# Performance work log

Hardware: AMD Instinct MI355X
Metric: run time of the kernel (lower is better)

Reference implementation:

```python
import jax, jax.numpy as jnp
import numpy as np

N_DIALOGS = 60
DIA_LEN = 100
N = N_DIALOGS * DIA_LEN  # 6000 utterances total
D_IN = 512
D_OUT = 512


def setup_inputs() -> dict:
    key = jax.random.key(0)
    k1, k2, k3, k4 = jax.random.split(key, 4)
    inputs = jax.random.normal(k1, (N, D_IN), dtype=jnp.float32)
    # per-dialog lengths (concrete host array; defines static graph structure)
    dia_len = np.full((N_DIALOGS,), DIA_LEN, dtype=np.int64)
    # one-hot speaker mask [N, 1, 2]; qmask[j,0,0]==1 -> speaker0 else speaker1
    sp = jax.random.randint(k2, (N,), 0, 2)
    qmask = jnp.zeros((N, 1, 2), jnp.int64).at[jnp.arange(N), 0, sp].set(1)
    W = jax.random.normal(k3, (D_OUT, D_IN), dtype=jnp.float32) / np.sqrt(D_IN)
    b = jax.random.normal(k4, (D_OUT,), dtype=jnp.float32) * 0.01
    return {"inputs": inputs, "dia_len": dia_len, "qmask": qmask, "W": W, "b": b}


def build_adj(inputs, dia_len, qmask):
    # Vectorized equivalent of message_passing_directed_speaker:
    # adj = I; edge (i,j) iff i,j in same dialog, same speaker, and consecutive
    # among that speaker's utterances; weight = 1 - arccos(clip(cos,-1,1))/pi.
    n = inputs.shape[0]
    dia_len_np = np.asarray(dia_len)
    did = jnp.asarray(np.repeat(np.arange(len(dia_len_np)), dia_len_np))  # dialog id per node
    sp0 = qmask[:, 0, 0] == 1  # True -> speaker0
    cs0 = jnp.cumsum(sp0.astype(jnp.int32))
    cs1 = jnp.cumsum((~sp0).astype(jnp.int32))
    csel = jnp.where(sp0, cs0, cs1)  # running count of own speaker
    idx = jnp.arange(n)
    # j>i, same dialog, same speaker, no same-speaker utterance strictly between
    upper = ((did[None, :] == did[:, None])
             & (sp0[None, :] == sp0[:, None])
             & (csel[None, :] - csel[:, None] == 1)
             & (idx[None, :] > idx[:, None]))
    edge = upper | upper.T
    # pairwise cosine similarity (cossim returns 0 when a norm is 0)
    nrm = jnp.sqrt(jnp.sum(inputs * inputs, axis=-1))  # [N]
    denom = nrm[:, None] * nrm[None, :]
    dots = inputs @ inputs.T  # [N, N]
    cos = jnp.where(denom > 0, dots / jnp.where(denom > 0, denom, 1.0), 0.0)
    cos_safe = jnp.where(edge, jnp.clip(cos, -1.0, 1.0), 0.0)
    w = 1.0 - jnp.arccos(cos_safe) / jnp.pi
    return jnp.where(edge, w, 0.0) + jnp.eye(n, dtype=inputs.dtype)


def reference(inputs, dia_len, qmask, W, b):
    adj = build_adj(inputs, dia_len, qmask)  # [N, N]
    x = adj @ inputs                          # [N, D_IN]
    return x @ W.T + b                        # [N, D_OUT]
```

## Files before the change

### kernel.cpp

```cpp
#include <hip/hip_runtime.h>
#include <hip/hip_bf16.h>

#define N_NODES 6000
#define N_DIA   60
#define DIA     100
#define DDIM    512
#define LDA     520

typedef short short8   __attribute__((ext_vector_type(8)));
typedef float floatx4  __attribute__((ext_vector_type(4)));

__device__ __forceinline__ unsigned short f2bf(float f) {
    unsigned int u = __float_as_uint(f);
    unsigned int r = (u + 0x7fffu + ((u >> 16) & 1u)) >> 16;
    return (unsigned short)r;
}

__device__ __forceinline__ float wave_reduce_sum(float v) {
    #pragma unroll
    for (int off = 32; off > 0; off >>= 1) v += __shfl_xor(v, off, 64);
    return v;
}

__global__ __launch_bounds__(256) void edge_kernel(
    const float* __restrict__ x, const int* __restrict__ qmask,
    const float* __restrict__ W, int* __restrict__ nxt, int* __restrict__ prv,
    float* __restrict__ wn, unsigned short* __restrict__ wbf)
{
    int bid = blockIdx.x;
    int tid = threadIdx.x;
    if (bid >= N_NODES / 4) {
        int base = (bid - N_NODES / 4) * 2048 + tid * 8;
        float4 a = *(const float4*)(W + base);
        float4 b = *(const float4*)(W + base + 4);
        union { unsigned short u[8]; short8 v; } o;
        o.u[0]=f2bf(a.x); o.u[1]=f2bf(a.y); o.u[2]=f2bf(a.z); o.u[3]=f2bf(a.w);
        o.u[4]=f2bf(b.x); o.u[5]=f2bf(b.y); o.u[6]=f2bf(b.z); o.u[7]=f2bf(b.w);
        *(short8*)(wbf + base) = o.v;
        return;
    }
    int wv = tid >> 6, lane = tid & 63;
    int i = bid * 4 + wv;
    int sp = qmask[2 * i];
    int dstart = (i / DIA) * DIA;
    int dend   = dstart + DIA;

    int cand = i + 1 + lane;
    unsigned long long b1 = __ballot(cand < dend && qmask[2 * cand] == sp);
    int j = -1;
    if (b1) j = i + __ffsll(b1);
    else {
        int c2 = i + 65 + lane;
        unsigned long long b2 = __ballot(lane < 35 && c2 < dend && qmask[2 * c2] == sp);
        if (b2) j = i + 64 + __ffsll(b2);
    }
    int candp = i - 1 - lane;
    unsigned long long p1 = __ballot(candp >= dstart && qmask[2 * candp] == sp);
    int p = -1;
    if (p1) p = i - __ffsll(p1);
    else {
        int pc2 = i - 65 - lane;
        unsigned long long p2 = __ballot(lane < 35 && pc2 >= dstart && qmask[2 * pc2] == sp);
        if (p2) p = i - 64 - __ffsll(p2);
    }

    float w = 0.0f;
    if (j >= 0) {
        const float* ri = x + (size_t)i * DDIM + lane * 8;
        const float* rj = x + (size_t)j * DDIM + lane * 8;
        float4 a0 = *(const float4*)(ri);
        float4 a1 = *(const float4*)(ri + 4);
        float4 b0 = *(const float4*)(rj);
        float4 b1 = *(const float4*)(rj + 4);
        float d  = a0.x*b0.x + a0.y*b0.y + a0.z*b0.z + a0.w*b0.w
                 + a1.x*b1.x + a1.y*b1.y + a1.z*b1.z + a1.w*b1.w;
        float ni = a0.x*a0.x + a0.y*a0.y + a0.z*a0.z + a0.w*a0.w
                 + a1.x*a1.x + a1.y*a1.y + a1.z*a1.z + a1.w*a1.w;
        float nj = b0.x*b0.x + b0.y*b0.y + b0.z*b0.z + b0.w*b0.w
                 + b1.x*b1.x + b1.y*b1.y + b1.z*b1.z + b1.w*b1.w;
        d  = wave_reduce_sum(d);
        ni = wave_reduce_sum(ni);
        nj = wave_reduce_sum(nj);
        float dn = ni * nj;
        float c = (dn > 0.0f) ? (d * __frsqrt_rn(dn)) : 0.0f;
        c = fminf(1.0f, fmaxf(-1.0f, c));
        w = 1.0f - acosf(c) * 0.3183098861837907f;
    }
    if (lane == 0) { nxt[i] = j; prv[i] = p; wn[i] = w; }
}

__global__ __launch_bounds__(512) void build_gemm(
    const float* __restrict__ x, const int* __restrict__ nxt,
    const int* __restrict__ prv, const float* __restrict__ wn,
    const unsigned short* __restrict__ wbf, const float* __restrict__ bias,
    float* __restrict__ out)
{
    __shared__ unsigned short As[64 * LDA];
    int tid = threadIdx.x;
    int wv = tid >> 6, lane = tid & 63;
    int m0 = blockIdx.x * 64;

    #pragma unroll 2
    for (int t = 0; t < 8; ++t) {
        int rr = wv * 8 + t;
        int i = m0 + rr;
        unsigned short* dst = As + rr * LDA + lane * 8;
        if (i >= N_NODES) {
            *(short8*)dst = (short8)0;
            continue;
        }
        int j = nxt[i];
        int p = prv[i];
        float wi = (j >= 0) ? wn[i] : 0.0f;
        float wp = (p >= 0) ? wn[p] : 0.0f;
        const float* ri = x + (size_t)i * DDIM + lane * 8;
        float acc[8];
        {
            float4 a = *(const float4*)(ri);
            float4 b = *(const float4*)(ri + 4);
            acc[0]=a.x; acc[1]=a.y; acc[2]=a.z; acc[3]=a.w;
            acc[4]=b.x; acc[5]=b.y; acc[6]=b.z; acc[7]=b.w;
        }
        if (j >= 0) {
            const float* rj = x + (size_t)j * DDIM + lane * 8;
            float4 a = *(const float4*)(rj);
            float4 b = *(const float4*)(rj + 4);
            acc[0]+=wi*a.x; acc[1]+=wi*a.y; acc[2]+=wi*a.z; acc[3]+=wi*a.w;
            acc[4]+=wi*b.x; acc[5]+=wi*b.y; acc[6]+=wi*b.z; acc[7]+=wi*b.w;
        }
        if (p >= 0) {
            const float* rp = x + (size_t)p * DDIM + lane * 8;
            float4 a = *(const float4*)(rp);
            float4 b = *(const float4*)(rp + 4);
            acc[0]+=wp*a.x; acc[1]+=wp*a.y; acc[2]+=wp*a.z; acc[3]+=wp*a.w;
            acc[4]+=wp*b.x; acc[5]+=wp*b.y; acc[6]+=wp*b.z; acc[7]+=wp*b.w;
        }
        union { unsigned short u[8]; short8 v; } o;
        #pragma unroll
        for (int q = 0; q < 8; ++q) o.u[q] = f2bf(acc[q]);
        *(short8*)dst = o.v;
    }
    __syncthreads();

    int n0 = blockIdx.y * 256 + wv * 32;
    int fr = lane & 15;
    int kq = (lane >> 4) * 8;
    floatx4 acc[4][2] = {};
    const unsigned short* As_base = As + fr * LDA + kq;
    const unsigned short* bb = wbf + (size_t)(n0 + fr) * DDIM + kq;

    #pragma unroll 2
    for (int k = 0; k < DDIM; k += 32) {
        short8 af[4], bfv[2];
        #pragma unroll
        for (int ms = 0; ms < 4; ++ms)
            af[ms] = *(const short8*)(As_base + ms * 16 * LDA + k);
        #pragma unroll
        for (int ns = 0; ns < 2; ++ns)
            bfv[ns] = *(const short8*)(bb + (size_t)ns * 16 * DDIM + k);
        #pragma unroll
        for (int ms = 0; ms < 4; ++ms)
            #pragma unroll
            for (int ns = 0; ns < 2; ++ns)
                acc[ms][ns] = __builtin_amdgcn_mfma_f32_16x16x32_bf16(
                    af[ms], bfv[ns], acc[ms][ns], 0, 0, 0);
    }

    int col = lane & 15;
    int rbase = (lane >> 4) * 4;
    #pragma unroll
    for (int ms = 0; ms < 4; ++ms) {
        #pragma unroll
        for (int ns = 0; ns < 2; ++ns) {
            int n = n0 + ns * 16 + col;
            float bv = bias[n];
            #pragma unroll
            for (int r = 0; r < 4; ++r) {
                int m = m0 + ms * 16 + rbase + r;
                if (m < N_NODES)
                    out[(size_t)m * DDIM + n] = acc[ms][ns][r] + bv;
            }
        }
    }
}

extern "C" void kernel_launch(void* const* d_in, const int* in_sizes, int n_in,
                              void* d_out, int out_size, void* d_ws, size_t ws_size,
                              hipStream_t stream) {
    const float* inputs = (const float*)d_in[0];
    const int* qmask   = (const int*)d_in[2];
    const float* W     = (const float*)d_in[3];
    const float* bias  = (const float*)d_in[4];
    float* out = (float*)d_out;

    char* ws = (char*)d_ws;
    unsigned short* wbf = (unsigned short*)ws;
    float* wn  = (float*)(ws + 524288);
    int*   nxt = (int*)(ws + 524288 + 24576);
    int*   prv = (int*)(ws + 524288 + 2 * 24576);

    edge_kernel<<<dim3(N_NODES / 4 + 128), 256, 0, stream>>>(
        inputs, qmask, W, nxt, prv, wn, wbf);
    build_gemm <<<dim3(94, 2),            512, 0, stream>>>(
        inputs, nxt, prv, wn, wbf, bias, out);
}
```

Before: 93.70 us.

## Fuse edge discovery and cosine weights into the build+GEMM kernel

Neighbour finding moves into the build+GEMM kernel: each block stages the speaker flags of its dialog range in shared memory and scans serially for next and previous same-speaker nodes. The cosine weights are then computed inline from the rows already loaded for aggregation. The old edge kernel, which read x for every node and wrote nxt/prv/wn through global memory, shrinks to a small W-cast kernel. This removes a large pass over x and the global round-trip, at the cost of recomputing each edge weight in both directions and doing the serial scans in one wave per block.

```diff
diff --git a/kernel.cpp b/kernel.cpp
--- a/kernel.cpp
+++ b/kernel.cpp
@@ -2,7 +2,6 @@
 #include <hip/hip_bf16.h>
 
 #define N_NODES 6000
-#define N_DIA   60
 #define DIA     100
 #define DDIM    512
 #define LDA     520
@@ -22,85 +21,54 @@
     return v;
 }
 
-__global__ __launch_bounds__(256) void edge_kernel(
+__global__ __launch_bounds__(512) void wcast_kernel(
+    const float* __restrict__ W, unsigned short* __restrict__ wbf)
+{
+    int base = blockIdx.x * 4096 + threadIdx.x * 8;
+    float4 a = *(const float4*)(W + base);
+    float4 b = *(const float4*)(W + base + 4);
+    union { unsigned short u[8]; short8 v; } o;
+    o.u[0]=f2bf(a.x); o.u[1]=f2bf(a.y); o.u[2]=f2bf(a.z); o.u[3]=f2bf(a.w);
+    o.u[4]=f2bf(b.x); o.u[5]=f2bf(b.y); o.u[6]=f2bf(b.z); o.u[7]=f2bf(b.w);
+    *(short8*)(wbf + base) = o.v;
+}
+
+__global__ __launch_bounds__(512) void fused_kernel(
     const float* __restrict__ x, const int* __restrict__ qmask,
-    const float* __restrict__ W, int* __restrict__ nxt, int* __restrict__ prv,
-    float* __restrict__ wn, unsigned short* __restrict__ wbf)
-{
-    int bid = blockIdx.x;
-    int tid = threadIdx.x;
-    if (bid >= N_NODES / 4) {
-        int base = (bid - N_NODES / 4) * 2048 + tid * 8;
-        float4 a = *(const float4*)(W + base);
-        float4 b = *(const float4*)(W + base + 4);
-        union { unsigned short u[8]; short8 v; } o;
-        o.u[0]=f2bf(a.x); o.u[1]=f2bf(a.y); o.u[2]=f2bf(a.z); o.u[3]=f2bf(a.w);
-        o.u[4]=f2bf(b.x); o.u[5]=f2bf(b.y); o.u[6]=f2bf(b.z); o.u[7]=f2bf(b.w);
-        *(short8*)(wbf + base) = o.v;
-        return;
-    }
-    int wv = tid >> 6, lane = tid & 63;
-    int i = bid * 4 + wv;
-    int sp = qmask[2 * i];
-    int dstart = (i / DIA) * DIA;
-    int dend   = dstart + DIA;
-
-    int cand = i + 1 + lane;
-    unsigned long long b1 = __ballot(cand < dend && qmask[2 * cand] == sp);
-    int j = -1;
-    if (b1) j = i + __ffsll(b1);
-    else {
-        int c2 = i + 65 + lane;
-        unsigned long long b2 = __ballot(lane < 35 && c2 < dend && qmask[2 * c2] == sp);
-        if (b2) j = i + 64 + __ffsll(b2);
-    }
-    int candp = i - 1 - lane;
-    unsigned long long p1 = __ballot(candp >= dstart && qmask[2 * candp] == sp);
-    int p = -1;
-    if (p1) p = i - __ffsll(p1);
-    else {
-        int pc2 = i - 65 - lane;
-        unsigned long long p2 = __ballot(lane < 35 && pc2 >= dstart && qmask[2 * pc2] == sp);
-        if (p2) p = i - 64 - __ffsll(p2);
-    }
-
-    float w = 0.0f;
-    if (j >= 0) {
-        const float* ri = x + (size_t)i * DDIM + lane * 8;
-        const float* rj = x + (size_t)j * DDIM + lane * 8;
-        float4 a0 = *(const float4*)(ri);
-        float4 a1 = *(const float4*)(ri + 4);
-        float4 b0 = *(const float4*)(rj);
-        float4 b1 = *(const float4*)(rj + 4);
-        float d  = a0.x*b0.x + a0.y*b0.y + a0.z*b0.z + a0.w*b0.w
-                 + a1.x*b1.x + a1.y*b1.y + a1.z*b1.z + a1.w*b1.w;
-        float ni = a0.x*a0.x + a0.y*a0.y + a0.z*a0.z + a0.w*a0.w
-                 + a1.x*a1.x + a1.y*a1.y + a1.z*a1.z + a1.w*a1.w;
-        float nj = b0.x*b0.x + b0.y*b0.y + b0.z*b0.z + b0.w*b0.w
-                 + b1.x*b1.x + b1.y*b1.y + b1.z*b1.z + b1.w*b1.w;
-        d  = wave_reduce_sum(d);
-        ni = wave_reduce_sum(ni);
-        nj = wave_reduce_sum(nj);
-        float dn = ni * nj;
-        float c = (dn > 0.0f) ? (d * __frsqrt_rn(dn)) : 0.0f;
-        c = fminf(1.0f, fmaxf(-1.0f, c));
-        w = 1.0f - acosf(c) * 0.3183098861837907f;
-    }
-    if (lane == 0) { nxt[i] = j; prv[i] = p; wn[i] = w; }
-}
-
-__global__ __launch_bounds__(512) void build_gemm(
-    const float* __restrict__ x, const int* __restrict__ nxt,
-    const int* __restrict__ prv, const float* __restrict__ wn,
     const unsigned short* __restrict__ wbf, const float* __restrict__ bias,
     float* __restrict__ out)
 {
     __shared__ unsigned short As[64 * LDA];
+    __shared__ int sp_s[200];
+    __shared__ int nxt_s[64];
+    __shared__ int prv_s[64];
+
     int tid = threadIdx.x;
     int wv = tid >> 6, lane = tid & 63;
     int m0 = blockIdx.x * 64;
 
-    #pragma unroll 2
+    int dia_lo = (m0 / DIA) * DIA;
+    int dia_hi = ((m0 + 63) / DIA) * DIA + DIA;
+    if (dia_hi > N_NODES) dia_hi = N_NODES;
+    int range = dia_hi - dia_lo;
+    if (tid < range) sp_s[tid] = qmask[2 * (dia_lo + tid)];
+    __syncthreads();
+
+    if (tid < 64) {
+        int i = m0 + tid;
+        int nx = -1, pv = -1;
+        if (i < N_NODES) {
+            int li = i - dia_lo;
+            int ds = (i / DIA) * DIA - dia_lo;
+            int de = ds + DIA;
+            int sp = sp_s[li];
+            for (int q = li + 1; q < de; ++q) if (sp_s[q] == sp) { nx = q + dia_lo; break; }
+            for (int q = li - 1; q >= ds; --q) if (sp_s[q] == sp) { pv = q + dia_lo; break; }
+        }
+        nxt_s[tid] = nx; prv_s[tid] = pv;
+    }
+    __syncthreads();
+
     for (int t = 0; t < 8; ++t) {
         int rr = wv * 8 + t;
         int i = m0 + rr;
@@ -109,31 +77,63 @@
             *(short8*)dst = (short8)0;
             continue;
         }
-        int j = nxt[i];
-        int p = prv[i];
-        float wi = (j >= 0) ? wn[i] : 0.0f;
-        float wp = (p >= 0) ? wn[p] : 0.0f;
+        int j = nxt_s[rr];
+        int p = prv_s[rr];
         const float* ri = x + (size_t)i * DDIM + lane * 8;
-        float acc[8];
-        {
-            float4 a = *(const float4*)(ri);
-            float4 b = *(const float4*)(ri + 4);
-            acc[0]=a.x; acc[1]=a.y; acc[2]=a.z; acc[3]=a.w;
-            acc[4]=b.x; acc[5]=b.y; acc[6]=b.z; acc[7]=b.w;
-        }
+        float4 xa = *(const float4*)(ri);
+        float4 xb = *(const float4*)(ri + 4);
+        float ni = xa.x*xa.x + xa.y*xa.y + xa.z*xa.z + xa.w*xa.w
+                 + xb.x*xb.x + xb.y*xb.y + xb.z*xb.z + xb.w*xb.w;
+        float dj = 0.0f, nj = 0.0f, dp = 0.0f, np = 0.0f;
+        float4 ja, jb, pa, pb;
         if (j >= 0) {
             const float* rj = x + (size_t)j * DDIM + lane * 8;
-            float4 a = *(const float4*)(rj);
-            float4 b = *(const float4*)(rj + 4);
-            acc[0]+=wi*a.x; acc[1]+=wi*a.y; acc[2]+=wi*a.z; acc[3]+=wi*a.w;
-            acc[4]+=wi*b.x; acc[5]+=wi*b.y; acc[6]+=wi*b.z; acc[7]+=wi*b.w;
+            ja = *(const float4*)(rj);
+            jb = *(const float4*)(rj + 4);
+            dj = xa.x*ja.x + xa.y*ja.y + xa.z*ja.z + xa.w*ja.w
+               + xb.x*jb.x + xb.y*jb.y + xb.z*jb.z + xb.w*jb.w;
+            nj = ja.x*ja.x + ja.y*ja.y + ja.z*ja.z + ja.w*ja.w
+               + jb.x*jb.x + jb.y*jb.y + jb.z*jb.z + jb.w*jb.w;
         }
         if (p >= 0) {
             const float* rp = x + (size_t)p * DDIM + lane * 8;
-            float4 a = *(const float4*)(rp);
-            float4 b = *(const float4*)(rp + 4);
-            acc[0]+=wp*a.x; acc[1]+=wp*a.y; acc[2]+=wp*a.z; acc[3]+=wp*a.w;
-            acc[4]+=wp*b.x; acc[5]+=wp*b.y; acc[6]+=wp*b.z; acc[7]+=wp*b.w;
+            pa = *(const float4*)(rp);
+            pb = *(const float4*)(rp + 4);
+            dp = xa.x*pa.x + xa.y*pa.y + xa.z*pa.z + xa.w*pa.w
+               + xb.x*pb.x + xb.y*pb.y + xb.z*pb.z + xb.w*pb.w;
+            np = pa.x*pa.x + pa.y*pa.y + pa.z*pa.z + pa.w*pa.w
+               + pb.x*pb.x + pb.y*pb.y + pb.z*pb.z + pb.w*pb.w;
+        }
+        ni = wave_reduce_sum(ni);
+        dj = wave_reduce_sum(dj);
+        nj = wave_reduce_sum(nj);
+        dp = wave_reduce_sum(dp);
+        np = wave_reduce_sum(np);
+
+        float wx = 0.0f, wp = 0.0f;
+        if (j >= 0) {
+            float dn = ni * nj;
+            float c = (dn > 0.0f) ? (dj * __frsqrt_rn(dn)) : 0.0f;
+            c = fminf(1.0f, fmaxf(-1.0f, c));
+            wx = 1.0f - acosf(c) * 0.3183098861837907f;
+        }
+        if (p >= 0) {
+            float dn = np * ni;
+            float c = (dn > 0.0f) ? (dp * __frsqrt_rn(dn)) : 0.0f;
+            c = fminf(1.0f, fmaxf(-1.0f, c));
+            wp = 1.0f - acosf(c) * 0.3183098861837907f;
+        }
+
+        float acc[8];
+        acc[0]=xa.x; acc[1]=xa.y; acc[2]=xa.z; acc[3]=xa.w;
+        acc[4]=xb.x; acc[5]=xb.y; acc[6]=xb.z; acc[7]=xb.w;
+        if (j >= 0) {
+            acc[0]+=wx*ja.x; acc[1]+=wx*ja.y; acc[2]+=wx*ja.z; acc[3]+=wx*ja.w;
+            acc[4]+=wx*jb.x; acc[5]+=wx*jb.y; acc[6]+=wx*jb.z; acc[7]+=wx*jb.w;
+        }
+        if (p >= 0) {
+            acc[0]+=wp*pa.x; acc[1]+=wp*pa.y; acc[2]+=wp*pa.z; acc[3]+=wp*pa.w;
+            acc[4]+=wp*pb.x; acc[5]+=wp*pb.y; acc[6]+=wp*pb.z; acc[7]+=wp*pb.w;
         }
         union { unsigned short u[8]; short8 v; } o;
         #pragma unroll
@@ -193,14 +193,8 @@
     const float* bias  = (const float*)d_in[4];
     float* out = (float*)d_out;
 
-    char* ws = (char*)d_ws;
-    unsigned short* wbf = (unsigned short*)ws;
-    float* wn  = (float*)(ws + 524288);
-    int*   nxt = (int*)(ws + 524288 + 24576);
-    int*   prv = (int*)(ws + 524288 + 2 * 24576);
-
-    edge_kernel<<<dim3(N_NODES / 4 + 128), 256, 0, stream>>>(
-        inputs, qmask, W, nxt, prv, wn, wbf);
-    build_gemm <<<dim3(94, 2),            512, 0, stream>>>(
-        inputs, nxt, prv, wn, wbf, bias, out);
-}
+    unsigned short* wbf = (unsigned short*)d_ws;
+
+    wcast_kernel<<<dim3(64),    512, 0, stream>>>(W, wbf);
+    fused_kernel<<<dim3(94, 2), 512, 0, stream>>>(inputs, qmask, wbf, bias, out);
+}
```

After: 95.83 us. 2.3% more time.
